# Kernel optimization log

Hardware: AMD Instinct MI355X
Metric: run time of the kernel (lower is better)

The kernel has to match this reference:

```python
import jax, jax.numpy as jnp
from jax import lax
import numpy as np

B, S, D = 32, 2048, 512

def setup_inputs() -> dict:
    key = jax.random.key(0)
    ks = jax.random.split(key, 9)
    inv = 1.0 / np.sqrt(D).astype(np.float32)
    return {
        "query": jax.random.normal(ks[0], (B, 1, D), jnp.float32),
        "value": jax.random.normal(ks[1], (B, S, D), jnp.float32),
        "last_alignment_energy": jax.random.uniform(ks[2], (B, S), jnp.float32),
        "conv_w": jax.random.normal(ks[3], (D, 1, 3), jnp.float32) * 0.1,  # Conv1d(1->D,k=3)
        "conv_b": jax.random.normal(ks[4], (D,), jnp.float32) * 0.01,
        "w_q": jax.random.normal(ks[5], (D, D), jnp.float32) * inv,  # applied as x @ w_q
        "w_v": jax.random.normal(ks[6], (D, D), jnp.float32) * inv,
        "bias": jax.random.uniform(ks[7], (D,), jnp.float32, minval=-0.1, maxval=0.1),
        "score_w": jax.random.normal(ks[8], (D,), jnp.float32) * inv,  # score_proj weight (out=1)
        "score_b": jnp.zeros((), jnp.float32),
    }


def reference(query, value, last_alignment_energy, conv_w, conv_b, w_q, w_v, bias, score_w, score_b):
    # location features: Conv1d(1->D, k=3, pad=1) over the previous alignment
    loc = lax.conv_general_dilated(
        last_alignment_energy[:, None, :], conv_w,
        window_strides=(1,), padding=[(1, 1)],
        dimension_numbers=("NCH", "OIH", "NCH"))  # [B, D, S]
    loc = jnp.transpose(loc, (0, 2, 1)) + conv_b  # [B, S, D]

    # additive attention energy: tanh(Wq q + Wv v + loc + b) @ score_w
    hidden = jnp.tanh(query @ w_q + value @ w_v + loc + bias)  # [B, S, D] (query broadcasts over S)
    scores = hidden @ score_w + score_b                          # [B, S]
    align = jax.nn.softmax(scores, axis=-1)                      # [B, S]

    # context = align^T V
    context = jnp.einsum("bs,bsd->bd", align, value)             # [B, D]
    return context, align
```

## Files before the change

kernel.cpp:

```cpp
#include <hip/hip_runtime.h>
#include <hip/hip_bf16.h>

#define B_ 32
#define S_ 2048
#define D_ 512
#define M_ (B_*S_)

typedef __bf16 bf16x8 __attribute__((ext_vector_type(8)));
typedef float  f32x4  __attribute__((ext_vector_type(4)));

__device__ __forceinline__ float tanh_fast(float x){
  float e2 = __expf(2.f * x);
  return 1.f - 2.f * __builtin_amdgcn_rcpf(e2 + 1.f);
}

__device__ __forceinline__ bf16x8 pack8(f32x4 r0, f32x4 r1){
  bf16x8 t;
  t[0]=(__bf16)r0[0]; t[1]=(__bf16)r0[1]; t[2]=(__bf16)r0[2]; t[3]=(__bf16)r0[3];
  t[4]=(__bf16)r1[0]; t[5]=(__bf16)r1[1]; t[6]=(__bf16)r1[2]; t[7]=(__bf16)r1[3];
  return t;
}

__device__ __forceinline__ void gl_lds16(const float* g, float* l){
  __builtin_amdgcn_global_load_lds(
      (const __attribute__((address_space(1))) void*)g,
      (__attribute__((address_space(3))) void*)l, 16, 0, 0);
}

__global__ void k_prep(const float* __restrict__ wv,
                       unsigned short* __restrict__ wvr,
                       const float* __restrict__ q,
                       const float* __restrict__ wq,
                       const float* __restrict__ bias,
                       float* __restrict__ qp){
  __shared__ float qs[D_];
  __shared__ float red2[2][128];
  int bid = blockIdx.x, t = threadIdx.x;
  if (bid < 128){
    int frag = bid*4 + (t>>6);
    int lane = t & 63;
    int ks = frag >> 5, nt = frag & 31;
    int k0 = ks*32 + (lane>>4)*8;
    int d  = nt*16 + (lane&15);
    bf16x8 v;
    #pragma unroll
    for (int j=0;j<8;++j) v[j] = (__bf16)wv[(k0+j)*D_ + d];
    *reinterpret_cast<uint4*>(wvr + ((size_t)frag*64 + lane)*8) =
        __builtin_bit_cast(uint4, v);
  } else {
    int idx = bid - 128;
    int b = idx >> 2, ch = idx & 3;
    int dl = t & 127, eg = t >> 7;
    int d  = ch*128 + dl;
    for (int e=t; e<D_; e+=256) qs[e] = q[b*D_+e];
    __syncthreads();
    float a = 0.f;
    #pragma unroll 8
    for (int i=0;i<256;++i){
      int e = eg*256 + i;
      a = fmaf(qs[e], wq[(size_t)e*D_+d], a);
    }
    red2[eg][dl] = a;
    __syncthreads();
    if (eg == 0) qp[b*D_+d] = red2[0][dl] + red2[1][dl] + bias[d];
  }
}

__launch_bounds__(256, 2)
__global__ void k_energy(const float* __restrict__ value,
                         const unsigned short* __restrict__ wvr,
                         const float* __restrict__ qp,
                         const float* __restrict__ energy,
                         const float* __restrict__ conv_w,
                         const float* __restrict__ conv_b,
                         const float* __restrict__ score_w,
                         float* __restrict__ scores){
  const int t    = threadIdx.x;
  const int wave = t >> 6;
  const int lane = t & 63;
  const int quad = lane >> 4;
  const int lm   = lane & 15;
  const int row0 = blockIdx.x * 32;
  const int b    = row0 >> 11;
  const int s0   = row0 & (S_-1);

  __shared__ __align__(16) float Af[32*512];

  #pragma unroll
  for (int i=0;i<16;++i){
    int j  = wave*16 + i;
    int r  = j >> 1;
    int x  = ((r&7)<<1) | ((r>>3)&1);
    int pg = ((j&1)<<6) | lane;
    gl_lds16(value + (size_t)(row0+r)*D_ + ((pg ^ x)<<2), &Af[j*256]);
  }

  f32x4 acc[2][8];
  #pragma unroll
  for (int mt=0;mt<2;++mt)
    #pragma unroll
    for (int n=0;n<8;++n)
      acc[mt][n] = (f32x4){0.f,0.f,0.f,0.f};

  const unsigned short* bP = wvr + ((size_t)(wave*8)*64 + lane)*8;
  bf16x8 bc[8];
  #pragma unroll
  for (int n=0;n<8;++n)
    bc[n] = __builtin_bit_cast(bf16x8,
        *reinterpret_cast<const uint4*>(bP + (size_t)n*512));

  __syncthreads();

  const int fl = ((lm&7)<<1) | (lm>>3);
  for (int c=0;c<16;++c){
    bf16x8 a[2];
    #pragma unroll
    for (int mt=0;mt<2;++mt){
      const float* base = &Af[(mt*16+lm)*512];
      int ga = (c*8 + quad*2) ^ fl;
      f32x4 r0 = *reinterpret_cast<const f32x4*>(base + ga*4);
      f32x4 r1 = *reinterpret_cast<const f32x4*>(base + (ga^1)*4);
      a[mt] = pack8(r0, r1);
    }
    __builtin_amdgcn_s_setprio(1);
    #pragma unroll
    for (int n=0;n<8;++n){
      bf16x8 bv = bc[n];
      if (c < 15)
        bc[n] = __builtin_bit_cast(bf16x8,
            *reinterpret_cast<const uint4*>(bP + (size_t)((c+1)*32+n)*512));
      acc[0][n] = __builtin_amdgcn_mfma_f32_16x16x32_bf16(a[0], bv, acc[0][n], 0,0,0);
      acc[1][n] = __builtin_amdgcn_mfma_f32_16x16x32_bf16(a[1], bv, acc[1][n], 0,0,0);
    }
    __builtin_amdgcn_s_setprio(0);
  }

  float sw[8], c0[8], c1[8], c2[8], cb[8], qv[8];
  #pragma unroll
  for (int n=0; n<8; ++n){
    int d = wave*128 + n*16 + lm;
    sw[n] = score_w[d];
    c0[n] = conv_w[d*3+0];
    c1[n] = conv_w[d*3+1];
    c2[n] = conv_w[d*3+2];
    cb[n] = conv_b[d];
    qv[n] = qp[b*D_+d];
  }
  __syncthreads();
  float* red = &Af[0];
  const float* eB = energy + b*S_;
  #pragma unroll
  for (int mt=0; mt<2; ++mt){
    #pragma unroll
    for (int r=0;r<4;++r){
      int sl = mt*16 + quad*4 + r;
      int s  = s0 + sl;
      float em1 = (s > 0)    ? eB[s-1] : 0.f;
      float e0  =              eB[s];
      float ep1 = (s < S_-1) ? eB[s+1] : 0.f;
      float p = 0.f;
      #pragma unroll
      for (int n=0; n<8; ++n){
        float h = acc[mt][n][r] + qv[n]
                + fmaf(c0[n],em1, fmaf(c1[n],e0, fmaf(c2[n],ep1, cb[n])));
        p = fmaf(sw[n], tanh_fast(h), p);
      }
      #pragma unroll
      for (int m=1; m<16; m<<=1) p += __shfl_xor(p, m, 64);
      if (lm == 0) red[wave*32 + sl] = p;
    }
  }
  __syncthreads();
  if (t < 32)
    scores[row0 + t] = red[t] + red[32+t] + red[64+t] + red[96+t];
}

__global__ void k_softmax(const float* __restrict__ sp,
                          const float* __restrict__ score_b,
                          float* __restrict__ out_align,
                          float* __restrict__ out_ctx){
  int b = blockIdx.x, t = threadIdx.x;
  int lane = t & 63, wid = t >> 6;
  out_ctx[b*D_ + t]       = 0.f;
  out_ctx[b*D_ + 256 + t] = 0.f;
  float sb = score_b[0];
  float v[8], mx = -3.4e38f;
  #pragma unroll
  for (int i=0;i<8;++i){
    float sc = sp[b*S_ + t + i*256] + sb;
    v[i] = sc;
    mx = fmaxf(mx, sc);
  }
  __shared__ float red[4], red2[4];
  #pragma unroll
  for (int m=1;m<64;m<<=1) mx = fmaxf(mx, __shfl_xor(mx, m, 64));
  if (lane==0) red[wid] = mx;
  __syncthreads();
  mx = fmaxf(fmaxf(red[0],red[1]), fmaxf(red[2],red[3]));
  float sum = 0.f;
  #pragma unroll
  for (int i=0;i<8;++i){ v[i] = __expf(v[i]-mx); sum += v[i]; }
  #pragma unroll
  for (int m=1;m<64;m<<=1) sum += __shfl_xor(sum, m, 64);
  if (lane==0) red2[wid] = sum;
  __syncthreads();
  sum = red2[0]+red2[1]+red2[2]+red2[3];
  float inv = 1.f/sum;
  #pragma unroll
  for (int i=0;i<8;++i) out_align[b*S_ + t + i*256] = v[i]*inv;
}

__global__ void k_ctx_part(const float* __restrict__ value,
                           const float* __restrict__ align,
                           float* __restrict__ out_ctx){
  int b = blockIdx.y, sc = blockIdx.x;
  int t = threadIdx.x;
  int r = t >> 7;
  int c = (t & 127) * 4;
  __shared__ float al[64];
  if (t < 64) al[t] = align[b*S_ + sc*64 + t];
  __syncthreads();
  f32x4 acc = (f32x4){0.f,0.f,0.f,0.f};
  const float* vbase = value + ((size_t)(b*S_ + sc*64 + r))*D_ + c;
  #pragma unroll 8
  for (int i=0;i<32;++i){
    f32x4 v = *reinterpret_cast<const f32x4*>(vbase + (size_t)(2*i)*D_);
    acc += al[2*i+r] * v;
  }
  __shared__ float lred[2][D_];
  #pragma unroll
  for (int j=0;j<4;++j) lred[r][c+j] = acc[j];
  __syncthreads();
  if (r == 0){
    #pragma unroll
    for (int j=0;j<4;++j)
      atomicAdd(&out_ctx[(size_t)b*D_ + c + j], lred[0][c+j] + lred[1][c+j]);
  }
}

extern "C" void kernel_launch(void* const* d_in, const int* in_sizes, int n_in,
                              void* d_out, int out_size, void* d_ws, size_t ws_size,
                              hipStream_t stream){
  const float* query   = (const float*)d_in[0];
  const float* value   = (const float*)d_in[1];
  const float* energy  = (const float*)d_in[2];
  const float* conv_w  = (const float*)d_in[3];
  const float* conv_b  = (const float*)d_in[4];
  const float* w_q     = (const float*)d_in[5];
  const float* w_v     = (const float*)d_in[6];
  const float* bias    = (const float*)d_in[7];
  const float* score_w = (const float*)d_in[8];
  const float* score_b = (const float*)d_in[9];

  char* ws = (char*)d_ws;
  unsigned short* wvr = (unsigned short*)(ws);
  float* qp    = (float*)(ws + (512<<10));
  float* sp    = (float*)(ws + (576<<10));

  float* out_ctx   = (float*)d_out;
  float* out_align = out_ctx + B_*D_;

  k_prep    <<<dim3(256),     dim3(256), 0, stream>>>(w_v, wvr, query, w_q, bias, qp);
  k_energy  <<<dim3(M_/32),   dim3(256), 0, stream>>>(value, wvr, qp, energy,
                                                      conv_w, conv_b, score_w, sp);
  k_softmax <<<dim3(B_),      dim3(256), 0, stream>>>(sp, score_b, out_align, out_ctx);
  k_ctx_part<<<dim3(32,B_),   dim3(256), 0, stream>>>(value, out_align, out_ctx);
}
```

Baseline: 293.5 us.

## Retile energy GEMM into 128x128 blocks with double-buffered LDS K-chunks

New measurement: 314.5 us. 1.07x slower.

```diff
diff --git a/kernel.cpp b/kernel.cpp
--- a/kernel.cpp
+++ b/kernel.cpp
@@ -21,7 +21,7 @@
   return t;
 }
 
-__device__ __forceinline__ void gl_lds16(const float* g, float* l){
+__device__ __forceinline__ void gl_lds16(const void* g, void* l){
   __builtin_amdgcn_global_load_lds(
       (const __attribute__((address_space(1))) void*)g,
       (__attribute__((address_space(3))) void*)l, 16, 0, 0);
@@ -66,7 +66,7 @@
   }
 }
 
-__launch_bounds__(256, 2)
+__launch_bounds__(256, 3)
 __global__ void k_energy(const float* __restrict__ value,
                          const unsigned short* __restrict__ wvr,
                          const float* __restrict__ qp,
@@ -74,71 +74,85 @@
                          const float* __restrict__ conv_w,
                          const float* __restrict__ conv_b,
                          const float* __restrict__ score_w,
-                         float* __restrict__ scores){
+                         float* __restrict__ sp){
   const int t    = threadIdx.x;
   const int wave = t >> 6;
   const int lane = t & 63;
   const int quad = lane >> 4;
   const int lm   = lane & 15;
-  const int row0 = blockIdx.x * 32;
+  const int w    = ((blockIdx.x & 7) << 8) | (blockIdx.x >> 3);
+  const int rp   = w >> 2;
+  const int cp   = w & 3;
+  const int row0 = rp * 128;
   const int b    = row0 >> 11;
   const int s0   = row0 & (S_-1);
 
-  __shared__ __align__(16) float Af[32*512];
-
-  #pragma unroll
-  for (int i=0;i<16;++i){
-    int j  = wave*16 + i;
-    int r  = j >> 1;
-    int x  = ((r&7)<<1) | ((r>>3)&1);
-    int pg = ((j&1)<<6) | lane;
-    gl_lds16(value + (size_t)(row0+r)*D_ + ((pg ^ x)<<2), &Af[j*256]);
-  }
-
-  f32x4 acc[2][8];
-  #pragma unroll
-  for (int mt=0;mt<2;++mt)
-    #pragma unroll
-    for (int n=0;n<8;++n)
+  __shared__ __align__(16) float          Abuf[2][4096];
+  __shared__ __align__(16) unsigned short Bbuf[2][4096];
+
+  int aoff[4];
+  #pragma unroll
+  for (int i=0;i<4;++i){
+    int j = wave*4 + i;
+    int r = j*8 + (lane>>3);
+    int p = lane & 7;
+    aoff[i] = (row0 + r)*D_ + (((p ^ (r&7)) << 2));
+  }
+  const int fb = cp*8 + wave*2;
+
+  f32x4 acc[4][4];
+  #pragma unroll
+  for (int mt=0;mt<4;++mt)
+    #pragma unroll
+    for (int n=0;n<4;++n)
       acc[mt][n] = (f32x4){0.f,0.f,0.f,0.f};
 
-  const unsigned short* bP = wvr + ((size_t)(wave*8)*64 + lane)*8;
-  bf16x8 bc[8];
-  #pragma unroll
-  for (int n=0;n<8;++n)
-    bc[n] = __builtin_bit_cast(bf16x8,
-        *reinterpret_cast<const uint4*>(bP + (size_t)n*512));
-
-  __syncthreads();
-
-  const int fl = ((lm&7)<<1) | (lm>>3);
+  const int mrow = (wave>>1)*64;
+  const int nco  = (wave&1)*4;
+
+  #pragma unroll
+  for (int i=0;i<4;++i)
+    gl_lds16(value + aoff[i], &Abuf[0][(wave*4+i)*256]);
+  #pragma unroll
+  for (int i=0;i<2;++i)
+    gl_lds16(wvr + (size_t)(fb+i)*512 + lane*8, &Bbuf[0][(wave*2+i)*512]);
+  __syncthreads();
+
   for (int c=0;c<16;++c){
-    bf16x8 a[2];
-    #pragma unroll
-    for (int mt=0;mt<2;++mt){
-      const float* base = &Af[(mt*16+lm)*512];
-      int ga = (c*8 + quad*2) ^ fl;
-      f32x4 r0 = *reinterpret_cast<const f32x4*>(base + ga*4);
-      f32x4 r1 = *reinterpret_cast<const f32x4*>(base + (ga^1)*4);
+    const int buf = c & 1;
+    if (c < 15){
+      #pragma unroll
+      for (int i=0;i<4;++i)
+        gl_lds16(value + aoff[i] + (c+1)*32, &Abuf[buf^1][(wave*4+i)*256]);
+      #pragma unroll
+      for (int i=0;i<2;++i)
+        gl_lds16(wvr + ((size_t)((c+1)*32 + fb + i))*512 + lane*8,
+                 &Bbuf[buf^1][(wave*2+i)*512]);
+    }
+    bf16x8 a[4], bq[4];
+    #pragma unroll
+    for (int mt=0;mt<4;++mt){
+      const float* Ab = &Abuf[buf][(mrow + mt*16 + lm)*32];
+      f32x4 r0 = *reinterpret_cast<const f32x4*>(Ab + ((((quad<<1)  ) ^ (lm&7))<<2));
+      f32x4 r1 = *reinterpret_cast<const f32x4*>(Ab + ((((quad<<1)|1) ^ (lm&7))<<2));
       a[mt] = pack8(r0, r1);
     }
-    __builtin_amdgcn_s_setprio(1);
-    #pragma unroll
-    for (int n=0;n<8;++n){
-      bf16x8 bv = bc[n];
-      if (c < 15)
-        bc[n] = __builtin_bit_cast(bf16x8,
-            *reinterpret_cast<const uint4*>(bP + (size_t)((c+1)*32+n)*512));
-      acc[0][n] = __builtin_amdgcn_mfma_f32_16x16x32_bf16(a[0], bv, acc[0][n], 0,0,0);
-      acc[1][n] = __builtin_amdgcn_mfma_f32_16x16x32_bf16(a[1], bv, acc[1][n], 0,0,0);
-    }
-    __builtin_amdgcn_s_setprio(0);
-  }
-
-  float sw[8], c0[8], c1[8], c2[8], cb[8], qv[8];
-  #pragma unroll
-  for (int n=0; n<8; ++n){
-    int d = wave*128 + n*16 + lm;
+    #pragma unroll
+    for (int n=0;n<4;++n)
+      bq[n] = __builtin_bit_cast(bf16x8,
+          *reinterpret_cast<const uint4*>(&Bbuf[buf][(nco+n)*512 + lane*8]));
+    #pragma unroll
+    for (int n=0;n<4;++n)
+      #pragma unroll
+      for (int mt=0;mt<4;++mt)
+        acc[mt][n] = __builtin_amdgcn_mfma_f32_16x16x32_bf16(a[mt], bq[n], acc[mt][n], 0,0,0);
+    __syncthreads();
+  }
+
+  float sw[4], c0[4], c1[4], c2[4], cb[4], qv[4];
+  #pragma unroll
+  for (int n=0; n<4; ++n){
+    int d = cp*128 + (wave&1)*64 + n*16 + lm;
     sw[n] = score_w[d];
     c0[n] = conv_w[d*3+0];
     c1[n] = conv_w[d*3+1];
@@ -146,33 +160,32 @@
     cb[n] = conv_b[d];
     qv[n] = qp[b*D_+d];
   }
-  __syncthreads();
-  float* red = &Af[0];
+  float* red = (float*)&Abuf[0][0];
   const float* eB = energy + b*S_;
   #pragma unroll
-  for (int mt=0; mt<2; ++mt){
+  for (int mt=0; mt<4; ++mt){
     #pragma unroll
     for (int r=0;r<4;++r){
-      int sl = mt*16 + quad*4 + r;
+      int sl = mrow + mt*16 + quad*4 + r;
       int s  = s0 + sl;
       float em1 = (s > 0)    ? eB[s-1] : 0.f;
       float e0  =              eB[s];
       float ep1 = (s < S_-1) ? eB[s+1] : 0.f;
       float p = 0.f;
       #pragma unroll
-      for (int n=0; n<8; ++n){
+      for (int n=0; n<4; ++n){
         float h = acc[mt][n][r] + qv[n]
                 + fmaf(c0[n],em1, fmaf(c1[n],e0, fmaf(c2[n],ep1, cb[n])));
         p = fmaf(sw[n], tanh_fast(h), p);
       }
       #pragma unroll
       for (int m=1; m<16; m<<=1) p += __shfl_xor(p, m, 64);
-      if (lm == 0) red[wave*32 + sl] = p;
-    }
-  }
-  __syncthreads();
-  if (t < 32)
-    scores[row0 + t] = red[t] + red[32+t] + red[64+t] + red[96+t];
+      if (lm == 0) red[(wave&1)*128 + sl] = p;
+    }
+  }
+  __syncthreads();
+  if (t < 128)
+    sp[(size_t)cp*M_ + row0 + t] = red[t] + red[128+t];
 }
 
 __global__ void k_softmax(const float* __restrict__ sp,
@@ -187,7 +200,8 @@
   float v[8], mx = -3.4e38f;
   #pragma unroll
   for (int i=0;i<8;++i){
-    float sc = sp[b*S_ + t + i*256] + sb;
+    int idx = b*S_ + t + i*256;
+    float sc = sp[idx] + sp[M_+idx] + sp[2*M_+idx] + sp[3*M_+idx] + sb;
     v[i] = sc;
     mx = fmaxf(mx, sc);
   }
@@ -260,9 +274,9 @@
   float* out_ctx   = (float*)d_out;
   float* out_align = out_ctx + B_*D_;
 
-  k_prep    <<<dim3(256),     dim3(256), 0, stream>>>(w_v, wvr, query, w_q, bias, qp);
-  k_energy  <<<dim3(M_/32),   dim3(256), 0, stream>>>(value, wvr, qp, energy,
-                                                      conv_w, conv_b, score_w, sp);
-  k_softmax <<<dim3(B_),      dim3(256), 0, stream>>>(sp, score_b, out_align, out_ctx);
-  k_ctx_part<<<dim3(32,B_),   dim3(256), 0, stream>>>(value, out_align, out_ctx);
-}
+  k_prep    <<<dim3(256),      dim3(256), 0, stream>>>(w_v, wvr, query, w_q, bias, qp);
+  k_energy  <<<dim3(M_/128*4), dim3(256), 0, stream>>>(value, wvr, qp, energy,
+                                                       conv_w, conv_b, score_w, sp);
+  k_softmax <<<dim3(B_),       dim3(256), 0, stream>>>(sp, score_b, out_align, out_ctx);
+  k_ctx_part<<<dim3(32,B_),    dim3(256), 0, stream>>>(value, out_align, out_ctx);
+}
```

## Retile energy GEMM to 256-row by 256-column blocks with LDS double-buffered weights

Applied to the files above, without the earlier changes.

After: 298.5 us. Within noise of the previous version (+1.7%).

```diff
diff --git a/kernel.cpp b/kernel.cpp
--- a/kernel.cpp
+++ b/kernel.cpp
@@ -21,7 +21,7 @@
   return t;
 }
 
-__device__ __forceinline__ void gl_lds16(const float* g, float* l){
+__device__ __forceinline__ void gl_lds16(const void* g, void* l){
   __builtin_amdgcn_global_load_lds(
       (const __attribute__((address_space(1))) void*)g,
       (__attribute__((address_space(3))) void*)l, 16, 0, 0);
@@ -66,7 +66,7 @@
   }
 }
 
-__launch_bounds__(256, 2)
+__launch_bounds__(512, 2)
 __global__ void k_energy(const float* __restrict__ value,
                          const unsigned short* __restrict__ wvr,
                          const float* __restrict__ qp,
@@ -74,71 +74,81 @@
                          const float* __restrict__ conv_w,
                          const float* __restrict__ conv_b,
                          const float* __restrict__ score_w,
-                         float* __restrict__ scores){
+                         float* __restrict__ sp){
   const int t    = threadIdx.x;
   const int wave = t >> 6;
   const int lane = t & 63;
   const int quad = lane >> 4;
   const int lm   = lane & 15;
-  const int row0 = blockIdx.x * 32;
+  const int wr   = wave >> 1;
+  const int wc   = wave & 1;
+  const int w    = ((blockIdx.x & 7) << 6) | (blockIdx.x >> 3);
+  const int rp   = w >> 1;
+  const int cp   = w & 1;
+  const int row0 = rp * 256;
   const int b    = row0 >> 11;
   const int s0   = row0 & (S_-1);
 
-  __shared__ __align__(16) float Af[32*512];
-
-  #pragma unroll
-  for (int i=0;i<16;++i){
-    int j  = wave*16 + i;
-    int r  = j >> 1;
-    int x  = ((r&7)<<1) | ((r>>3)&1);
-    int pg = ((j&1)<<6) | lane;
-    gl_lds16(value + (size_t)(row0+r)*D_ + ((pg ^ x)<<2), &Af[j*256]);
-  }
-
-  f32x4 acc[2][8];
-  #pragma unroll
-  for (int mt=0;mt<2;++mt)
+  __shared__ __align__(16) unsigned short Blds[2][64*512];
+
+  const float* pA[4];
+  #pragma unroll
+  for (int mt=0;mt<4;++mt)
+    pA[mt] = value + (size_t)(row0 + wr*64 + mt*16 + lm)*D_ + quad*8;
+
+  f32x4 acc[4][8];
+  #pragma unroll
+  for (int mt=0;mt<4;++mt)
     #pragma unroll
     for (int n=0;n<8;++n)
       acc[mt][n] = (f32x4){0.f,0.f,0.f,0.f};
 
-  const unsigned short* bP = wvr + ((size_t)(wave*8)*64 + lane)*8;
-  bf16x8 bc[8];
-  #pragma unroll
-  for (int n=0;n<8;++n)
-    bc[n] = __builtin_bit_cast(bf16x8,
-        *reinterpret_cast<const uint4*>(bP + (size_t)n*512));
-
-  __syncthreads();
-
-  const int fl = ((lm&7)<<1) | (lm>>3);
-  for (int c=0;c<16;++c){
-    bf16x8 a[2];
-    #pragma unroll
-    for (int mt=0;mt<2;++mt){
-      const float* base = &Af[(mt*16+lm)*512];
-      int ga = (c*8 + quad*2) ^ fl;
-      f32x4 r0 = *reinterpret_cast<const f32x4*>(base + ga*4);
-      f32x4 r1 = *reinterpret_cast<const f32x4*>(base + (ga^1)*4);
-      a[mt] = pack8(r0, r1);
+  #pragma unroll
+  for (int i=0;i<8;++i){
+    int j  = wave*8 + i;
+    int gf = ((j>>4))*32 + cp*16 + (j&15);
+    gl_lds16(wvr + (size_t)gf*512 + lane*8, &Blds[0][j*512]);
+  }
+  __syncthreads();
+
+  for (int q4=0; q4<4; ++q4){
+    const int buf = q4 & 1;
+    #pragma unroll
+    for (int c=0;c<4;++c){
+      const int gc = q4*4 + c;
+      bf16x8 a[4];
+      #pragma unroll
+      for (int mt=0;mt<4;++mt){
+        f32x4 r0 = *reinterpret_cast<const f32x4*>(pA[mt] + gc*32);
+        f32x4 r1 = *reinterpret_cast<const f32x4*>(pA[mt] + gc*32 + 4);
+        a[mt] = pack8(r0, r1);
+      }
+      __builtin_amdgcn_s_setprio(1);
+      #pragma unroll
+      for (int n=0;n<8;++n){
+        bf16x8 bq = __builtin_bit_cast(bf16x8,
+            *reinterpret_cast<const uint4*>(&Blds[buf][(c*16 + wc*8 + n)*512 + lane*8]));
+        #pragma unroll
+        for (int mt=0;mt<4;++mt)
+          acc[mt][n] = __builtin_amdgcn_mfma_f32_16x16x32_bf16(a[mt], bq, acc[mt][n], 0,0,0);
+      }
+      __builtin_amdgcn_s_setprio(0);
+      if (c == 0 && q4 < 3){
+        #pragma unroll
+        for (int i=0;i<8;++i){
+          int j  = wave*8 + i;
+          int gf = ((q4+1)*4 + (j>>4))*32 + cp*16 + (j&15);
+          gl_lds16(wvr + (size_t)gf*512 + lane*8, &Blds[buf^1][j*512]);
+        }
+      }
     }
-    __builtin_amdgcn_s_setprio(1);
-    #pragma unroll
-    for (int n=0;n<8;++n){
-      bf16x8 bv = bc[n];
-      if (c < 15)
-        bc[n] = __builtin_bit_cast(bf16x8,
-            *reinterpret_cast<const uint4*>(bP + (size_t)((c+1)*32+n)*512));
-      acc[0][n] = __builtin_amdgcn_mfma_f32_16x16x32_bf16(a[0], bv, acc[0][n], 0,0,0);
-      acc[1][n] = __builtin_amdgcn_mfma_f32_16x16x32_bf16(a[1], bv, acc[1][n], 0,0,0);
-    }
-    __builtin_amdgcn_s_setprio(0);
+    __syncthreads();
   }
 
   float sw[8], c0[8], c1[8], c2[8], cb[8], qv[8];
   #pragma unroll
   for (int n=0; n<8; ++n){
-    int d = wave*128 + n*16 + lm;
+    int d = cp*256 + wc*128 + n*16 + lm;
     sw[n] = score_w[d];
     c0[n] = conv_w[d*3+0];
     c1[n] = conv_w[d*3+1];
@@ -146,14 +156,13 @@
     cb[n] = conv_b[d];
     qv[n] = qp[b*D_+d];
   }
-  __syncthreads();
-  float* red = &Af[0];
+  float* red = (float*)&Blds[0][0];
   const float* eB = energy + b*S_;
   #pragma unroll
-  for (int mt=0; mt<2; ++mt){
+  for (int mt=0; mt<4; ++mt){
     #pragma unroll
     for (int r=0;r<4;++r){
-      int sl = mt*16 + quad*4 + r;
+      int sl = wr*64 + mt*16 + quad*4 + r;
       int s  = s0 + sl;
       float em1 = (s > 0)    ? eB[s-1] : 0.f;
       float e0  =              eB[s];
@@ -167,12 +176,12 @@
       }
       #pragma unroll
       for (int m=1; m<16; m<<=1) p += __shfl_xor(p, m, 64);
-      if (lm == 0) red[wave*32 + sl] = p;
+      if (lm == 0) red[wc*256 + sl] = p;
     }
   }
   __syncthreads();
-  if (t < 32)
-    scores[row0 + t] = red[t] + red[32+t] + red[64+t] + red[96+t];
+  if (t < 256)
+    sp[(size_t)cp*M_ + row0 + t] = red[t] + red[256+t];
 }
 
 __global__ void k_softmax(const float* __restrict__ sp,
@@ -187,7 +196,8 @@
   float v[8], mx = -3.4e38f;
   #pragma unroll
   for (int i=0;i<8;++i){
-    float sc = sp[b*S_ + t + i*256] + sb;
+    int idx = b*S_ + t + i*256;
+    float sc = sp[idx] + sp[M_+idx] + sb;
     v[i] = sc;
     mx = fmaxf(mx, sc);
   }
@@ -260,9 +270,9 @@
   float* out_ctx   = (float*)d_out;
   float* out_align = out_ctx + B_*D_;
 
-  k_prep    <<<dim3(256),     dim3(256), 0, stream>>>(w_v, wvr, query, w_q, bias, qp);
-  k_energy  <<<dim3(M_/32),   dim3(256), 0, stream>>>(value, wvr, qp, energy,
-                                                      conv_w, conv_b, score_w, sp);
-  k_softmax <<<dim3(B_),      dim3(256), 0, stream>>>(sp, score_b, out_align, out_ctx);
-  k_ctx_part<<<dim3(32,B_),   dim3(256), 0, stream>>>(value, out_align, out_ctx);
-}
+  k_prep    <<<dim3(256),   dim3(256), 0, stream>>>(w_v, wvr, query, w_q, bias, qp);
+  k_energy  <<<dim3(512),   dim3(512), 0, stream>>>(value, wvr, qp, energy,
+                                                    conv_w, conv_b, score_w, sp);
+  k_softmax <<<dim3(B_),    dim3(256), 0, stream>>>(sp, score_b, out_align, out_ctx);
+  k_ctx_part<<<dim3(32,B_), dim3(256), 0, stream>>>(value, out_align, out_ctx);
+}
```
